# Performance work log

Measured on AMD Instinct MI355X. Metric: run time of the kernel, lower is better.

Reference implementation:

```python
import jax, jax.numpy as jnp
import numpy as np

N_NODES = 65536
IN_FEAT = 512
OUT_FEAT = 256
N_REL = 3
N_EDGES = 500000
NEG_SLOPE = 0.2  # DGL GATConv default
EPS = 1e-9


def setup_inputs() -> dict:
    key = jax.random.key(0)
    ks = jax.random.split(key, 7)
    h = jax.random.normal(ks[0], (N_NODES, IN_FEAT), dtype=jnp.float32)
    # Glorot-ish scaling keeps attention logits in a sane range
    W = jax.random.normal(ks[1], (N_REL, IN_FEAT, OUT_FEAT), dtype=jnp.float32) / np.sqrt(IN_FEAT)
    attn_l = jax.random.normal(ks[2], (N_REL, OUT_FEAT), dtype=jnp.float32) / np.sqrt(OUT_FEAT)
    attn_r = jax.random.normal(ks[3], (N_REL, OUT_FEAT), dtype=jnp.float32) / np.sqrt(OUT_FEAT)
    b = jnp.zeros((N_REL, OUT_FEAT), dtype=jnp.float32)
    src = jax.random.randint(ks[4], (N_REL, N_EDGES), 0, N_NODES, dtype=jnp.int32)
    dst = jax.random.randint(ks[5], (N_REL, N_EDGES), 0, N_NODES, dtype=jnp.int32)
    return {"h": h, "W": W, "attn_l": attn_l, "attn_r": attn_r, "b": b, "src": src, "dst": dst}


def _gat_relation(h, W_r, al_r, ar_r, b_r, src_r, dst_r):
    n = h.shape[0]
    z = h @ W_r                                  # [N, F_out] dense projection
    el = z @ al_r                                # [N] per-node left logit
    er = z @ ar_r                                # [N] per-node right logit
    e = jax.nn.leaky_relu(el[src_r] + er[dst_r], NEG_SLOPE)  # [E]
    # edge_softmax over incoming edges of each destination node
    m = jax.ops.segment_max(e, dst_r, num_segments=n)        # [N]
    w = jnp.exp(e - m[dst_r])                                # [E]
    denom = jax.ops.segment_sum(w, dst_r, num_segments=n)    # [N]
    alpha = w / (denom[dst_r] + EPS)                         # [E]
    out = jax.ops.segment_sum(alpha[:, None] * z[src_r], dst_r, num_segments=n)
    return out + b_r


def reference(h, W, attn_l, attn_r, b, src, dst):
    n_rel = W.shape[0]
    out = jnp.zeros((h.shape[0], W.shape[2]), dtype=h.dtype)
    # HeteroGraphConv default aggregate='sum' over relations; num_heads=1 then squeeze
    for r in range(n_rel):
        out = out + _gat_relation(h, W[r], attn_l[r], attn_r[r], b[r], src[r], dst[r])
    return out
```

## Files before the change

kernel.cpp:

```cpp
#include <hip/hip_runtime.h>
#include <hip/hip_bf16.h>
#include <cstdint>
#include <cstddef>

#define N_NODES 65536
#define IN_FEAT 512
#define OUT_FEAT 256
#define N_REL 3
#define TOT_EDGES (N_REL * 500000)
#define N_EDGES 500000
#define NEG_SLOPE 0.2f
#define EPS_F 1e-9f
#define BK 64

typedef __bf16 bf16x8 __attribute__((ext_vector_type(8)));
typedef float f32x4 __attribute__((ext_vector_type(4)));

__device__ __forceinline__ void async16(const void* g, void* l) {
    __builtin_amdgcn_global_load_lds(
        (const __attribute__((address_space(1))) unsigned int*)g,
        (__attribute__((address_space(3))) unsigned int*)l, 16, 0, 0);
}

__global__ void kInit(float* __restrict__ el, float* __restrict__ er,
                      int* __restrict__ head) {
    int i = blockIdx.x * blockDim.x + threadIdx.x;
    if (i < N_REL * N_NODES) {
        el[i] = 0.f;
        er[i] = 0.f;
        head[i] = -1;
    }
}

__global__ void kHb(const float* __restrict__ h, __bf16* __restrict__ hb) {
    int i = blockIdx.x * blockDim.x + threadIdx.x;
    const float4* src = (const float4*)h + (size_t)i * 2;
    float4 v0 = src[0], v1 = src[1];
    bf16x8 w;
    w[0] = (__bf16)v0.x; w[1] = (__bf16)v0.y; w[2] = (__bf16)v0.z; w[3] = (__bf16)v0.w;
    w[4] = (__bf16)v1.x; w[5] = (__bf16)v1.y; w[6] = (__bf16)v1.z; w[7] = (__bf16)v1.w;
    *(bf16x8*)(hb + (size_t)i * 8) = w;
}

__global__ __launch_bounds__(256) void kWt(const float* __restrict__ W, __bf16* __restrict__ Wt) {
    __shared__ float tile[64][65];
    int b = blockIdx.x;
    int r = b >> 5;
    int kt = (b >> 2) & 7;
    int nt = b & 3;
    int k0 = kt * 64, n0 = nt * 64;
    int t = threadIdx.x;
    int trow = t >> 6, tcol = t & 63;
    const float* Wr = W + (size_t)r * IN_FEAT * OUT_FEAT;
#pragma unroll
    for (int p = 0; p < 16; p++) {
        int k = p * 4 + trow;
        tile[k][tcol] = Wr[(size_t)(k0 + k) * OUT_FEAT + n0 + tcol];
    }
    __syncthreads();
    __bf16* Wtr = Wt + (size_t)r * OUT_FEAT * IN_FEAT;
#pragma unroll
    for (int p = 0; p < 16; p++) {
        int n = p * 4 + trow;
        Wtr[(size_t)(n0 + n) * IN_FEAT + k0 + tcol] = (__bf16)tile[tcol][n];
    }
}

__global__ __launch_bounds__(256, 2) void kGemmA(
    const __bf16* __restrict__ hb, const __bf16* __restrict__ Wt,
    const float* __restrict__ attn_l, const float* __restrict__ attn_r,
    __bf16* __restrict__ z, float* __restrict__ el, float* __restrict__ er) {
    __shared__ __bf16 Al[128 * BK];
    __shared__ __bf16 Bl[256 * BK];
    const int r = blockIdx.y;
    const int t = threadIdx.x;
    const int lane = t & 63;
    const int wave = t >> 6;
    const int wm = wave >> 1, wn = wave & 1;
    const int colL = lane & 15, quad = lane >> 4;
    const int m_base = blockIdx.x * 128;

    const __bf16* WtR = Wt + (size_t)r * OUT_FEAT * IN_FEAT;

    f32x4 acc[4][8];
#pragma unroll
    for (int mt = 0; mt < 4; mt++)
#pragma unroll
        for (int nt = 0; nt < 8; nt++) acc[mt][nt] = (f32x4){0.f, 0.f, 0.f, 0.f};

    for (int k0 = 0; k0 < IN_FEAT; k0 += BK) {
        if (k0) __syncthreads();
#pragma unroll
        for (int i = 0; i < 8; i++) {
            int s = i * 256 + t;
            int n = s >> 3, cp = s & 7, cs = cp ^ (n & 7);
            const __bf16* g = WtR + (size_t)n * IN_FEAT + k0 + cs * 8;
            __bf16* l = Bl + (size_t)(i * 256 + (wave << 6)) * 8;
            async16(g, l);
        }
#pragma unroll
        for (int i = 0; i < 4; i++) {
            int s = i * 256 + t;
            int row = s >> 3, cp = s & 7, cs = cp ^ (row & 7);
            const __bf16* g = hb + (size_t)(m_base + row) * IN_FEAT + k0 + cs * 8;
            __bf16* l = Al + (size_t)(i * 256 + (wave << 6)) * 8;
            async16(g, l);
        }
        __syncthreads();
#pragma unroll
        for (int kk = 0; kk < 2; kk++) {
            const int cbase = kk * 4 + quad;
            bf16x8 af[4], bfr[8];
#pragma unroll
            for (int mt = 0; mt < 4; mt++) {
                int row = wm * 64 + mt * 16 + colL;
                int cp = cbase ^ (row & 7);
                af[mt] = *(const bf16x8*)(Al + (size_t)((row << 3) + cp) * 8);
            }
#pragma unroll
            for (int nt = 0; nt < 8; nt++) {
                int n = wn * 128 + nt * 16 + colL;
                int cp = cbase ^ (n & 7);
                bfr[nt] = *(const bf16x8*)(Bl + (size_t)((n << 3) + cp) * 8);
            }
#pragma unroll
            for (int mt = 0; mt < 4; mt++)
#pragma unroll
                for (int nt = 0; nt < 8; nt++)
                    acc[mt][nt] = __builtin_amdgcn_mfma_f32_16x16x32_bf16(
                        af[mt], bfr[nt], acc[mt][nt], 0, 0, 0);
        }
    }

    const float* alv = attn_l + r * OUT_FEAT;
    const float* arv = attn_r + r * OUT_FEAT;
    __bf16* zr = z + (size_t)r * N_NODES * OUT_FEAT;
    float elp[4][4], erp[4][4];
#pragma unroll
    for (int mt = 0; mt < 4; mt++)
#pragma unroll
        for (int q = 0; q < 4; q++) { elp[mt][q] = 0.f; erp[mt][q] = 0.f; }
#pragma unroll
    for (int mt = 0; mt < 4; mt++) {
#pragma unroll
        for (int nt = 0; nt < 8; nt++) {
            int c = wn * 128 + nt * 16 + colL;
            float al = alv[c], ar = arv[c];
#pragma unroll
            for (int q = 0; q < 4; q++) {
                float v = acc[mt][nt][q];
                int row = m_base + wm * 64 + mt * 16 + quad * 4 + q;
                zr[(size_t)row * OUT_FEAT + c] = (__bf16)v;
                elp[mt][q] += v * al;
                erp[mt][q] += v * ar;
            }
        }
    }
#pragma unroll
    for (int mt = 0; mt < 4; mt++)
#pragma unroll
        for (int q = 0; q < 4; q++) {
#pragma unroll
            for (int off = 1; off < 16; off <<= 1) {
                elp[mt][q] += __shfl_xor(elp[mt][q], off, 64);
                erp[mt][q] += __shfl_xor(erp[mt][q], off, 64);
            }
        }
    if (colL == 0) {
#pragma unroll
        for (int mt = 0; mt < 4; mt++)
#pragma unroll
            for (int q = 0; q < 4; q++) {
                int row = m_base + wm * 64 + mt * 16 + quad * 4 + q;
                atomicAdd(el + r * N_NODES + row, elp[mt][q]);
                atomicAdd(er + r * N_NODES + row, erp[mt][q]);
            }
    }
}

__global__ __launch_bounds__(256) void kGemmC(
    const float* __restrict__ h, const __bf16* __restrict__ Wt,
    const float* __restrict__ attn_l, const float* __restrict__ attn_r,
    __bf16* __restrict__ z, float* __restrict__ el, float* __restrict__ er) {
    __shared__ __bf16 Al[128 * BK];
    __shared__ __bf16 Bl[256 * BK];
    const int r = blockIdx.y;
    const int t = threadIdx.x;
    const int lane = t & 63;
    const int wave = t >> 6;
    const int wm = wave >> 1, wn = wave & 1;
    const int colL = lane & 15, quad = lane >> 4;
    const int m_base = blockIdx.x * 128;
    const __bf16* WtR = Wt + (size_t)r * OUT_FEAT * IN_FEAT;

    f32x4 acc[4][8];
#pragma unroll
    for (int mt = 0; mt < 4; mt++)
#pragma unroll
        for (int nt = 0; nt < 8; nt++) acc[mt][nt] = (f32x4){0.f, 0.f, 0.f, 0.f};

    for (int k0 = 0; k0 < IN_FEAT; k0 += BK) {
        if (k0) __syncthreads();
#pragma unroll
        for (int i = 0; i < 8; i++) {
            int s = i * 256 + t;
            int n = s >> 3, cp = s & 7, cs = cp ^ (n & 7);
            const __bf16* g = WtR + (size_t)n * IN_FEAT + k0 + cs * 8;
            __bf16* l = Bl + (size_t)(i * 256 + (wave << 6)) * 8;
            async16(g, l);
        }
#pragma unroll
        for (int i = 0; i < 4; i++) {
            int s = i * 256 + t;
            int row = s >> 3, cp = s & 7, cs = cp ^ (row & 7);
            const float* g = h + (size_t)(m_base + row) * IN_FEAT + k0 + cs * 8;
            float4 v0 = ((const float4*)g)[0];
            float4 v1 = ((const float4*)g)[1];
            bf16x8 w;
            w[0] = (__bf16)v0.x; w[1] = (__bf16)v0.y; w[2] = (__bf16)v0.z; w[3] = (__bf16)v0.w;
            w[4] = (__bf16)v1.x; w[5] = (__bf16)v1.y; w[6] = (__bf16)v1.z; w[7] = (__bf16)v1.w;
            *(bf16x8*)(Al + (size_t)s * 8) = w;
        }
        __syncthreads();
#pragma unroll
        for (int kk = 0; kk < 2; kk++) {
            const int cbase = kk * 4 + quad;
            bf16x8 af[4], bfr[8];
#pragma unroll
            for (int mt = 0; mt < 4; mt++) {
                int row = wm * 64 + mt * 16 + colL;
                int cp = cbase ^ (row & 7);
                af[mt] = *(const bf16x8*)(Al + (size_t)((row << 3) + cp) * 8);
            }
#pragma unroll
            for (int nt = 0; nt < 8; nt++) {
                int n = wn * 128 + nt * 16 + colL;
                int cp = cbase ^ (n & 7);
                bfr[nt] = *(const bf16x8*)(Bl + (size_t)((n << 3) + cp) * 8);
            }
#pragma unroll
            for (int mt = 0; mt < 4; mt++)
#pragma unroll
                for (int nt = 0; nt < 8; nt++)
                    acc[mt][nt] = __builtin_amdgcn_mfma_f32_16x16x32_bf16(
                        af[mt], bfr[nt], acc[mt][nt], 0, 0, 0);
        }
    }
    const float* alv = attn_l + r * OUT_FEAT;
    const float* arv = attn_r + r * OUT_FEAT;
    __bf16* zr = z + (size_t)r * N_NODES * OUT_FEAT;
    float elp[4][4], erp[4][4];
#pragma unroll
    for (int mt = 0; mt < 4; mt++)
#pragma unroll
        for (int q = 0; q < 4; q++) { elp[mt][q] = 0.f; erp[mt][q] = 0.f; }
#pragma unroll
    for (int mt = 0; mt < 4; mt++) {
#pragma unroll
        for (int nt = 0; nt < 8; nt++) {
            int c = wn * 128 + nt * 16 + colL;
            float al = alv[c], ar = arv[c];
#pragma unroll
            for (int q = 0; q < 4; q++) {
                float v = acc[mt][nt][q];
                int row = m_base + wm * 64 + mt * 16 + quad * 4 + q;
                zr[(size_t)row * OUT_FEAT + c] = (__bf16)v;
                elp[mt][q] += v * al;
                erp[mt][q] += v * ar;
            }
        }
    }
#pragma unroll
    for (int mt = 0; mt < 4; mt++)
#pragma unroll
        for (int q = 0; q < 4; q++) {
#pragma unroll
            for (int off = 1; off < 16; off <<= 1) {
                elp[mt][q] += __shfl_xor(elp[mt][q], off, 64);
                erp[mt][q] += __shfl_xor(erp[mt][q], off, 64);
            }
        }
    if (colL == 0) {
#pragma unroll
        for (int mt = 0; mt < 4; mt++)
#pragma unroll
            for (int q = 0; q < 4; q++) {
                int row = m_base + wm * 64 + mt * 16 + quad * 4 + q;
                atomicAdd(el + r * N_NODES + row, elp[mt][q]);
                atomicAdd(er + r * N_NODES + row, erp[mt][q]);
            }
    }
}

__global__ void kLink(const int* __restrict__ dst, int* __restrict__ head,
                      int* __restrict__ next) {
    int i = blockIdx.x * blockDim.x + threadIdx.x;
    if (i >= TOT_EDGES) return;
    int r = i / N_EDGES;
    int d = dst[i];
    next[i] = atomicExch(head + r * N_NODES + d, i);
}

__global__ __launch_bounds__(256) void kAgg(
    const __bf16* __restrict__ z, const int* __restrict__ head,
    const int* __restrict__ next, const int* __restrict__ srcArr,
    const float* __restrict__ el, const float* __restrict__ er,
    const float* __restrict__ bias, float* __restrict__ out) {
    const int t = threadIdx.x;
    const int lane = t & 63;
    const int half = lane >> 5;
    const int l = lane & 31;
    const int node = blockIdx.x * 8 + (t >> 6) * 2 + half;
    const int c = l * 8;

    float f0, f1, f2, f3, f4, f5, f6, f7;
    {
        const float* b0 = bias + c;
        const float* b1 = bias + OUT_FEAT + c;
        const float* b2 = bias + 2 * OUT_FEAT + c;
        f0 = b0[0] + b1[0] + b2[0];
        f1 = b0[1] + b1[1] + b2[1];
        f2 = b0[2] + b1[2] + b2[2];
        f3 = b0[3] + b1[3] + b2[3];
        f4 = b0[4] + b1[4] + b2[4];
        f5 = b0[5] + b1[5] + b2[5];
        f6 = b0[6] + b1[6] + b2[6];
        f7 = b0[7] + b1[7] + b2[7];
    }

#pragma unroll
    for (int r = 0; r < N_REL; r++) {
        const int idx = r * N_NODES + node;
        const float erv = er[idx];
        const float* elr = el + r * N_NODES;
        const uint4* zrel = (const uint4*)(z + (size_t)r * N_NODES * OUT_FEAT);
        float p0 = 0.f, p1 = 0.f, p2 = 0.f, p3 = 0.f;
        float p4 = 0.f, p5 = 0.f, p6 = 0.f, p7 = 0.f;
        float wsum = 0.f;
        int cur = head[idx];
        while (cur >= 0) {
            int nx = next[cur];
            int s = srcArr[cur];
            float x = elr[s] + erv;
            x = x > 0.f ? x : NEG_SLOPE * x;
            float w = __expf(x);
            uint4 v = zrel[(size_t)s * 32 + l];
            wsum += w;
            p0 += w * __uint_as_float(v.x << 16);
            p1 += w * __uint_as_float(v.x & 0xFFFF0000u);
            p2 += w * __uint_as_float(v.y << 16);
            p3 += w * __uint_as_float(v.y & 0xFFFF0000u);
            p4 += w * __uint_as_float(v.z << 16);
            p5 += w * __uint_as_float(v.z & 0xFFFF0000u);
            p6 += w * __uint_as_float(v.w << 16);
            p7 += w * __uint_as_float(v.w & 0xFFFF0000u);
            cur = nx;
        }
        float invd = 1.f / (wsum + EPS_F);
        f0 += p0 * invd; f1 += p1 * invd; f2 += p2 * invd; f3 += p3 * invd;
        f4 += p4 * invd; f5 += p5 * invd; f6 += p6 * invd; f7 += p7 * invd;
    }

    float* orow = out + (size_t)node * OUT_FEAT + c;
    *(float4*)orow = make_float4(f0, f1, f2, f3);
    *(float4*)(orow + 4) = make_float4(f4, f5, f6, f7);
}

extern "C" void kernel_launch(void* const* d_in, const int* in_sizes, int n_in,
                              void* d_out, int out_size, void* d_ws, size_t ws_size,
                              hipStream_t stream) {
    const float* h      = (const float*)d_in[0];
    const float* W      = (const float*)d_in[1];
    const float* attn_l = (const float*)d_in[2];
    const float* attn_r = (const float*)d_in[3];
    const float* bias   = (const float*)d_in[4];
    const int*   src    = (const int*)d_in[5];
    const int*   dst    = (const int*)d_in[6];
    float* out = (float*)d_out;
    char* ws = (char*)d_ws;

    const bool useHb = ws_size >= (size_t)190000000;
    size_t off_b = 0;
    auto alloc = [&](size_t bytes) {
        size_t o = off_b;
        off_b = (off_b + bytes + 255) & ~(size_t)255;
        return o;
    };
    size_t oZ    = alloc((size_t)N_REL * N_NODES * OUT_FEAT * 2);
    size_t oHB   = useHb ? alloc((size_t)N_NODES * IN_FEAT * 2) : 0;
    size_t oWT   = alloc((size_t)N_REL * OUT_FEAT * IN_FEAT * 2);
    size_t oEL   = alloc((size_t)N_REL * N_NODES * 4);
    size_t oER   = alloc((size_t)N_REL * N_NODES * 4);
    size_t oHEAD = alloc((size_t)N_REL * N_NODES * 4);
    size_t oNEXT = alloc((size_t)TOT_EDGES * 4);

    __bf16* z    = (__bf16*)(ws + oZ);
    __bf16* hb   = (__bf16*)(ws + oHB);
    __bf16* Wt   = (__bf16*)(ws + oWT);
    float*  el   = (float*)(ws + oEL);
    float*  er   = (float*)(ws + oER);
    int*    head = (int*)(ws + oHEAD);
    int*    next = (int*)(ws + oNEXT);

    kInit<<<(N_REL * N_NODES + 255) / 256, 256, 0, stream>>>(el, er, head);
    kWt<<<96, 256, 0, stream>>>(W, Wt);
    kLink<<<(TOT_EDGES + 255) / 256, 256, 0, stream>>>(dst, head, next);
    if (useHb) {
        kHb<<<(N_NODES * IN_FEAT / 8 + 255) / 256, 256, 0, stream>>>(h, hb);
        kGemmA<<<dim3(N_NODES / 128, N_REL), 256, 0, stream>>>(hb, Wt, attn_l, attn_r, z, el, er);
    } else {
        kGemmC<<<dim3(N_NODES / 128, N_REL), 256, 0, stream>>>(h, Wt, attn_l, attn_r, z, el, er);
    }
    kAgg<<<N_NODES / 8, 256, 0, stream>>>(z, head, next, src, el, er, bias, out);
}
```

Baseline: 533.3 us.

## Walk each relation's edge list in parallel and pack next/src into int2

The aggregation kernel now gives each relation of a node its own half-wave, so the three linked-list walks for a node run concurrently instead of one after another. The per-relation results are combined through shared memory after a block barrier. The link kernel also stores the next pointer and the source index together as an int2, so each list step needs one dependent load instead of two. The costs are 8-byte next entries, a __syncthreads per block, and two-thirds of the threads sitting idle during the final reduction.

```diff
diff --git a/kernel.cpp b/kernel.cpp
--- a/kernel.cpp
+++ b/kernel.cpp
@@ -292,78 +292,85 @@
     }
 }
 
-__global__ void kLink(const int* __restrict__ dst, int* __restrict__ head,
-                      int* __restrict__ next) {
+__global__ void kLink(const int* __restrict__ dst, const int* __restrict__ srcArr,
+                      int* __restrict__ head, int2* __restrict__ next2) {
     int i = blockIdx.x * blockDim.x + threadIdx.x;
     if (i >= TOT_EDGES) return;
     int r = i / N_EDGES;
     int d = dst[i];
-    next[i] = atomicExch(head + r * N_NODES + d, i);
-}
-
-__global__ __launch_bounds__(256) void kAgg(
+    int prev = atomicExch(head + r * N_NODES + d, i);
+    next2[i] = make_int2(prev, srcArr[i]);
+}
+
+__global__ __launch_bounds__(192) void kAgg(
     const __bf16* __restrict__ z, const int* __restrict__ head,
-    const int* __restrict__ next, const int* __restrict__ srcArr,
+    const int2* __restrict__ next2,
     const float* __restrict__ el, const float* __restrict__ er,
     const float* __restrict__ bias, float* __restrict__ out) {
+    __shared__ float cm[6][256];
     const int t = threadIdx.x;
+    const int wv = t >> 6;
     const int lane = t & 63;
     const int half = lane >> 5;
     const int l = lane & 31;
-    const int node = blockIdx.x * 8 + (t >> 6) * 2 + half;
-    const int c = l * 8;
-
-    float f0, f1, f2, f3, f4, f5, f6, f7;
-    {
+    const int hw = wv * 2 + half;
+    const int nl = (hw >= 3) ? 1 : 0;
+    const int r = hw - nl * 3;
+    const int node = blockIdx.x * 2 + nl;
+    const int idx = r * N_NODES + node;
+
+    const float erv = er[idx];
+    const float* elr = el + r * N_NODES;
+    const uint4* zrel = (const uint4*)(z + (size_t)r * N_NODES * OUT_FEAT);
+
+    float p0 = 0.f, p1 = 0.f, p2 = 0.f, p3 = 0.f;
+    float p4 = 0.f, p5 = 0.f, p6 = 0.f, p7 = 0.f;
+    float wsum = 0.f;
+    int cur = head[idx];
+    while (cur >= 0) {
+        int2 ns = next2[cur];
+        int s = ns.y;
+        float x = elr[s] + erv;
+        x = x > 0.f ? x : NEG_SLOPE * x;
+        float w = __expf(x);
+        uint4 v = zrel[(size_t)s * 32 + l];
+        wsum += w;
+        p0 += w * __uint_as_float(v.x << 16);
+        p1 += w * __uint_as_float(v.x & 0xFFFF0000u);
+        p2 += w * __uint_as_float(v.y << 16);
+        p3 += w * __uint_as_float(v.y & 0xFFFF0000u);
+        p4 += w * __uint_as_float(v.z << 16);
+        p5 += w * __uint_as_float(v.z & 0xFFFF0000u);
+        p6 += w * __uint_as_float(v.w << 16);
+        p7 += w * __uint_as_float(v.w & 0xFFFF0000u);
+        cur = ns.x;
+    }
+    float invd = 1.f / (wsum + EPS_F);
+    float* cr = &cm[hw][l * 8];
+    *(float4*)cr       = make_float4(p0 * invd, p1 * invd, p2 * invd, p3 * invd);
+    *(float4*)(cr + 4) = make_float4(p4 * invd, p5 * invd, p6 * invd, p7 * invd);
+    __syncthreads();
+
+    if (r == 0) {
+        const int c = l * 8;
+        const float* r0 = &cm[nl * 3 + 0][c];
+        const float* r1 = &cm[nl * 3 + 1][c];
+        const float* r2 = &cm[nl * 3 + 2][c];
         const float* b0 = bias + c;
         const float* b1 = bias + OUT_FEAT + c;
         const float* b2 = bias + 2 * OUT_FEAT + c;
-        f0 = b0[0] + b1[0] + b2[0];
-        f1 = b0[1] + b1[1] + b2[1];
-        f2 = b0[2] + b1[2] + b2[2];
-        f3 = b0[3] + b1[3] + b2[3];
-        f4 = b0[4] + b1[4] + b2[4];
-        f5 = b0[5] + b1[5] + b2[5];
-        f6 = b0[6] + b1[6] + b2[6];
-        f7 = b0[7] + b1[7] + b2[7];
-    }
-
-#pragma unroll
-    for (int r = 0; r < N_REL; r++) {
-        const int idx = r * N_NODES + node;
-        const float erv = er[idx];
-        const float* elr = el + r * N_NODES;
-        const uint4* zrel = (const uint4*)(z + (size_t)r * N_NODES * OUT_FEAT);
-        float p0 = 0.f, p1 = 0.f, p2 = 0.f, p3 = 0.f;
-        float p4 = 0.f, p5 = 0.f, p6 = 0.f, p7 = 0.f;
-        float wsum = 0.f;
-        int cur = head[idx];
-        while (cur >= 0) {
-            int nx = next[cur];
-            int s = srcArr[cur];
-            float x = elr[s] + erv;
-            x = x > 0.f ? x : NEG_SLOPE * x;
-            float w = __expf(x);
-            uint4 v = zrel[(size_t)s * 32 + l];
-            wsum += w;
-            p0 += w * __uint_as_float(v.x << 16);
-            p1 += w * __uint_as_float(v.x & 0xFFFF0000u);
-            p2 += w * __uint_as_float(v.y << 16);
-            p3 += w * __uint_as_float(v.y & 0xFFFF0000u);
-            p4 += w * __uint_as_float(v.z << 16);
-            p5 += w * __uint_as_float(v.z & 0xFFFF0000u);
-            p6 += w * __uint_as_float(v.w << 16);
-            p7 += w * __uint_as_float(v.w & 0xFFFF0000u);
-            cur = nx;
-        }
-        float invd = 1.f / (wsum + EPS_F);
-        f0 += p0 * invd; f1 += p1 * invd; f2 += p2 * invd; f3 += p3 * invd;
-        f4 += p4 * invd; f5 += p5 * invd; f6 += p6 * invd; f7 += p7 * invd;
-    }
-
-    float* orow = out + (size_t)node * OUT_FEAT + c;
-    *(float4*)orow = make_float4(f0, f1, f2, f3);
-    *(float4*)(orow + 4) = make_float4(f4, f5, f6, f7);
+        float f0 = r0[0] + r1[0] + r2[0] + b0[0] + b1[0] + b2[0];
+        float f1 = r0[1] + r1[1] + r2[1] + b0[1] + b1[1] + b2[1];
+        float f2 = r0[2] + r1[2] + r2[2] + b0[2] + b1[2] + b2[2];
+        float f3 = r0[3] + r1[3] + r2[3] + b0[3] + b1[3] + b2[3];
+        float f4 = r0[4] + r1[4] + r2[4] + b0[4] + b1[4] + b2[4];
+        float f5 = r0[5] + r1[5] + r2[5] + b0[5] + b1[5] + b2[5];
+        float f6 = r0[6] + r1[6] + r2[6] + b0[6] + b1[6] + b2[6];
+        float f7 = r0[7] + r1[7] + r2[7] + b0[7] + b1[7] + b2[7];
+        float* orow = out + (size_t)node * OUT_FEAT + c;
+        *(float4*)orow       = make_float4(f0, f1, f2, f3);
+        *(float4*)(orow + 4) = make_float4(f4, f5, f6, f7);
+    }
 }
 
 extern "C" void kernel_launch(void* const* d_in, const int* in_sizes, int n_in,
@@ -392,7 +399,7 @@
     size_t oEL   = alloc((size_t)N_REL * N_NODES * 4);
     size_t oER   = alloc((size_t)N_REL * N_NODES * 4);
     size_t oHEAD = alloc((size_t)N_REL * N_NODES * 4);
-    size_t oNEXT = alloc((size_t)TOT_EDGES * 4);
+    size_t oNEXT = alloc((size_t)TOT_EDGES * 8);
 
     __bf16* z    = (__bf16*)(ws + oZ);
     __bf16* hb   = (__bf16*)(ws + oHB);
@@ -400,16 +407,16 @@
     float*  el   = (float*)(ws + oEL);
     float*  er   = (float*)(ws + oER);
     int*    head = (int*)(ws + oHEAD);
-    int*    next = (int*)(ws + oNEXT);
+    int2*   next2 = (int2*)(ws + oNEXT);
 
     kInit<<<(N_REL * N_NODES + 255) / 256, 256, 0, stream>>>(el, er, head);
     kWt<<<96, 256, 0, stream>>>(W, Wt);
-    kLink<<<(TOT_EDGES + 255) / 256, 256, 0, stream>>>(dst, head, next);
+    kLink<<<(TOT_EDGES + 255) / 256, 256, 0, stream>>>(dst, src, head, next2);
     if (useHb) {
         kHb<<<(N_NODES * IN_FEAT / 8 + 255) / 256, 256, 0, stream>>>(h, hb);
         kGemmA<<<dim3(N_NODES / 128, N_REL), 256, 0, stream>>>(hb, Wt, attn_l, attn_r, z, el, er);
     } else {
         kGemmC<<<dim3(N_NODES / 128, N_REL), 256, 0, stream>>>(h, Wt, attn_l, attn_r, z, el, er);
     }
-    kAgg<<<N_NODES / 8, 256, 0, stream>>>(z, head, next, src, el, er, bias, out);
-}
+    kAgg<<<N_NODES / 2, 192, 0, stream>>>(z, head, next2, el, er, bias, out);
+}
```

New measurement: 521.2 us. 2.3% less time.
